# Kernel optimization log

Measured on AMD Instinct MI355X. Metric: run time of the kernel, lower is better.

Reference implementation:

```python
import jax, jax.numpy as jnp
import numpy as np

THETA = 10000.0

def _angles(h, w, fpt):
    # base_angles: theta^{-linspace(0,1,1+fpt//4)[:-1]}  -> (fpt//4,)
    powers = jnp.linspace(0.0, 1.0, 1 + fpt // 4)[:-1]
    base = jnp.power(THETA, -powers)
    x_mults = jnp.tile(jnp.arange(w, dtype=base.dtype), h)            # (N,)
    y_mults = jnp.repeat(jnp.arange(h, dtype=base.dtype), w)          # (N,)
    ang_x = x_mults[:, None] * base                                   # (N, fpt//4)
    ang_y = y_mults[:, None] * base                                   # (N, fpt//4)
    return jnp.concatenate([ang_x, ang_y], axis=1)                    # (N, fpt//2)


def _rotate(t, cos, sin):
    # t: (b, h, n, c) -> pairs (b, h, n, c//2, 2); standard 2D rotation per pair.
    b, hh, n, c = t.shape
    v = t.reshape(b, hh, n, c // 2, 2)
    v0, v1 = v[..., 0], v[..., 1]
    o0 = cos * v0 - sin * v1
    o1 = sin * v0 + cos * v1
    return jnp.stack([o0, o1], axis=-1).reshape(b, hh, n, c)


def setup_inputs() -> dict:
    key = jax.random.key(0)
    kq, kk = jax.random.split(key)
    b, heads, n, c = 4, 4, 4096, 256
    return {
        "q": jax.random.normal(kq, (b, heads, n, c), dtype=jnp.float32),
        "k": jax.random.normal(kk, (b, heads, n, c), dtype=jnp.float32),
        "h": 64,
        "w": 64,
    }


def reference(q, k, h, w):
    c = q.shape[-1]
    ang = _angles(h, w, c)            # (N, c//2)
    cos, sin = jnp.cos(ang), jnp.sin(ang)
    q_out = _rotate(q, cos, sin)
    k_out = _rotate(k, cos, sin)      # nk == nq here (no tiling branch)
    return q_out, k_out
```

## Files before the change

kernel.cpp:

```cpp
#include <hip/hip_runtime.h>

constexpr int B_ = 4, H_ = 4, N_ = 4096, C_ = 256;
constexpr long long TENS = (long long)B_ * H_ * N_ * C_;
constexpr int VEC = 4;
constexpr long long NTHREADS = TENS / VEC;
constexpr int F4_PER_POS = C_ / 4;
constexpr int TAB_ENTRIES = N_ * F4_PER_POS;
constexpr size_t TAB_BYTES = (size_t)TAB_ENTRIES * 16;

typedef float f32x4 __attribute__((ext_vector_type(4)));

__device__ __forceinline__ unsigned read_w(const int* __restrict__ wp) {
    int wi = wp[0];
    if (wi <= 0 || wi > 65536) {
        float wf = __int_as_float(wi);
        wi = (wf > 0.0f && wf <= 65536.0f) ? (int)wf : 64;
    }
    return (unsigned)wi;
}

__global__ __launch_bounds__(256) void build_tab_kernel(
    const int* __restrict__ wp, f32x4* __restrict__ tab)
{
    const unsigned idx = blockIdx.x * 256 + threadIdx.x;
    const unsigned w = read_w(wp);
    const unsigned pos = idx >> 6;
    const unsigned fq  = idx & 63;
    const unsigned x = pos % w;
    const unsigned y = pos / w;
    const float mult = (fq < 32) ? (float)x : (float)y;
    const int f0 = (int)(2u * (fq & 31u));
    constexpr float NEG_LOG2_THETA_OVER_64 = -0.20762050593045494f;
    float c0, s0, c1, s1;
    sincosf(mult * exp2f((float)f0       * NEG_LOG2_THETA_OVER_64), &s0, &c0);
    sincosf(mult * exp2f((float)(f0 + 1) * NEG_LOG2_THETA_OVER_64), &s1, &c1);
    f32x4 v; v.x = c0; v.y = s0; v.z = c1; v.w = s1;
    tab[idx] = v;
}

__global__ __launch_bounds__(256) void rope2d_tab_kernel(
    const f32x4* __restrict__ q4,
    const f32x4* __restrict__ k4,
    const f32x4* __restrict__ tab,
    f32x4* __restrict__ oq4,
    f32x4* __restrict__ ok4)
{
    const unsigned t = blockIdx.x * 256 + threadIdx.x;
    const f32x4 cs = tab[t & (unsigned)(TAB_ENTRIES - 1)];
    const f32x4 qa = __builtin_nontemporal_load(&q4[t]);
    const f32x4 ka = __builtin_nontemporal_load(&k4[t]);

    f32x4 r;
    r.x = fmaf(cs.x, qa.x, -cs.y * qa.y);
    r.y = fmaf(cs.y, qa.x,  cs.x * qa.y);
    r.z = fmaf(cs.z, qa.z, -cs.w * qa.w);
    r.w = fmaf(cs.w, qa.z,  cs.z * qa.w);
    __builtin_nontemporal_store(r, &oq4[t]);

    r.x = fmaf(cs.x, ka.x, -cs.y * ka.y);
    r.y = fmaf(cs.y, ka.x,  cs.x * ka.y);
    r.z = fmaf(cs.z, ka.z, -cs.w * ka.w);
    r.w = fmaf(cs.w, ka.z,  cs.z * ka.w);
    __builtin_nontemporal_store(r, &ok4[t]);
}

__global__ __launch_bounds__(256) void rope2d_inline_kernel(
    const float4* __restrict__ q4,
    const float4* __restrict__ k4,
    const int* __restrict__ wp,
    float4* __restrict__ oq4,
    float4* __restrict__ ok4)
{
    const unsigned w = read_w(wp);
    const unsigned t = blockIdx.x * 256 + threadIdx.x;
    const unsigned e = t * VEC;

    const int cidx = (int)(e & (C_ - 1));
    const unsigned pos = (e >> 8) & (N_ - 1);
    const unsigned x = pos % w;
    const unsigned y = pos / w;

    const int j0 = cidx >> 1;
    const float mult = (j0 < C_ / 4) ? (float)x : (float)y;
    const int f0 = j0 & (C_ / 4 - 1);

    float cs0, sn0, cs1, sn1;
    sincosf(mult * exp2f((float)(f0    ) * (-0.20762050593045494f)), &sn0, &cs0);
    sincosf(mult * exp2f((float)(f0 + 1) * (-0.20762050593045494f)), &sn1, &cs1);

    const float4 qa = q4[t];
    const float4 ka = k4[t];

    float4 r;
    r.x = fmaf(cs0, qa.x, -sn0 * qa.y);  r.y = fmaf(sn0, qa.x, cs0 * qa.y);
    r.z = fmaf(cs1, qa.z, -sn1 * qa.w);  r.w = fmaf(sn1, qa.z, cs1 * qa.w);
    oq4[t] = r;

    r.x = fmaf(cs0, ka.x, -sn0 * ka.y);  r.y = fmaf(sn0, ka.x, cs0 * ka.y);
    r.z = fmaf(cs1, ka.z, -sn1 * ka.w);  r.w = fmaf(sn1, ka.z, cs1 * ka.w);
    ok4[t] = r;
}

extern "C" void kernel_launch(void* const* d_in, const int* in_sizes, int n_in,
                              void* d_out, int out_size, void* d_ws, size_t ws_size,
                              hipStream_t stream) {
    const int* wp = (const int*)d_in[3];
    float* out = (float*)d_out;

    if (d_ws != nullptr && ws_size >= TAB_BYTES) {
        f32x4* tab = (f32x4*)d_ws;
        build_tab_kernel<<<dim3(TAB_ENTRIES / 256), 256, 0, stream>>>(wp, tab);
        rope2d_tab_kernel<<<dim3((unsigned)(NTHREADS / 256)), 256, 0, stream>>>(
            (const f32x4*)d_in[0], (const f32x4*)d_in[1], tab,
            (f32x4*)out, (f32x4*)(out + TENS));
    } else {
        rope2d_inline_kernel<<<dim3((unsigned)(NTHREADS / 256)), 256, 0, stream>>>(
            (const float4*)d_in[0], (const float4*)d_in[1], wp,
            (float4*)out, (float4*)(out + TENS));
    }
}
```

Baseline: 226.2 us.

## Fuse angle table build into rope kernel and loop over batch-heads

Replaces the two-kernel plan (build a cos/sin table in workspace, then apply it) with a single kernel. Each thread computes its cos/sin values in registers once and loops over all 16 batch-head slabs. This removes the table write and read traffic and one kernel launch. In exchange the grid shrinks 16x to 1024 blocks, which lowers the parallelism available to hide memory latency in this bandwidth-bound kernel.

Result: no change. 229.8 us (+1.6%).

```diff
diff --git a/kernel.cpp b/kernel.cpp
--- a/kernel.cpp
+++ b/kernel.cpp
@@ -2,11 +2,10 @@
 
 constexpr int B_ = 4, H_ = 4, N_ = 4096, C_ = 256;
 constexpr long long TENS = (long long)B_ * H_ * N_ * C_;
-constexpr int VEC = 4;
-constexpr long long NTHREADS = TENS / VEC;
+constexpr int BH = B_ * H_;
 constexpr int F4_PER_POS = C_ / 4;
-constexpr int TAB_ENTRIES = N_ * F4_PER_POS;
-constexpr size_t TAB_BYTES = (size_t)TAB_ENTRIES * 16;
+constexpr unsigned SLAB_F4 = (unsigned)(N_ * F4_PER_POS);
+constexpr unsigned NIDX = SLAB_F4;
 
 typedef float f32x4 __attribute__((ext_vector_type(4)));
 
@@ -19,8 +18,12 @@
     return (unsigned)wi;
 }
 
-__global__ __launch_bounds__(256) void build_tab_kernel(
-    const int* __restrict__ wp, f32x4* __restrict__ tab)
+__global__ __launch_bounds__(256) void rope2d_fused_kernel(
+    const f32x4* __restrict__ q4,
+    const f32x4* __restrict__ k4,
+    const int* __restrict__ wp,
+    f32x4* __restrict__ oq4,
+    f32x4* __restrict__ ok4)
 {
     const unsigned idx = blockIdx.x * 256 + threadIdx.x;
     const unsigned w = read_w(wp);
@@ -28,77 +31,34 @@
     const unsigned fq  = idx & 63;
     const unsigned x = pos % w;
     const unsigned y = pos / w;
+
     const float mult = (fq < 32) ? (float)x : (float)y;
     const int f0 = (int)(2u * (fq & 31u));
+
     constexpr float NEG_LOG2_THETA_OVER_64 = -0.20762050593045494f;
     float c0, s0, c1, s1;
     sincosf(mult * exp2f((float)f0       * NEG_LOG2_THETA_OVER_64), &s0, &c0);
     sincosf(mult * exp2f((float)(f0 + 1) * NEG_LOG2_THETA_OVER_64), &s1, &c1);
-    f32x4 v; v.x = c0; v.y = s0; v.z = c1; v.w = s1;
-    tab[idx] = v;
-}
 
-__global__ __launch_bounds__(256) void rope2d_tab_kernel(
-    const f32x4* __restrict__ q4,
-    const f32x4* __restrict__ k4,
-    const f32x4* __restrict__ tab,
-    f32x4* __restrict__ oq4,
-    f32x4* __restrict__ ok4)
-{
-    const unsigned t = blockIdx.x * 256 + threadIdx.x;
-    const f32x4 cs = tab[t & (unsigned)(TAB_ENTRIES - 1)];
-    const f32x4 qa = __builtin_nontemporal_load(&q4[t]);
-    const f32x4 ka = __builtin_nontemporal_load(&k4[t]);
+    #pragma unroll 4
+    for (int bh = 0; bh < BH; ++bh) {
+        const unsigned t = (unsigned)bh * SLAB_F4 + idx;
+        const f32x4 qa = __builtin_nontemporal_load(&q4[t]);
+        const f32x4 ka = __builtin_nontemporal_load(&k4[t]);
 
-    f32x4 r;
-    r.x = fmaf(cs.x, qa.x, -cs.y * qa.y);
-    r.y = fmaf(cs.y, qa.x,  cs.x * qa.y);
-    r.z = fmaf(cs.z, qa.z, -cs.w * qa.w);
-    r.w = fmaf(cs.w, qa.z,  cs.z * qa.w);
-    __builtin_nontemporal_store(r, &oq4[t]);
+        f32x4 r;
+        r.x = fmaf(c0, qa.x, -s0 * qa.y);
+        r.y = fmaf(s0, qa.x,  c0 * qa.y);
+        r.z = fmaf(c1, qa.z, -s1 * qa.w);
+        r.w = fmaf(s1, qa.z,  c1 * qa.w);
+        __builtin_nontemporal_store(r, &oq4[t]);
 
-    r.x = fmaf(cs.x, ka.x, -cs.y * ka.y);
-    r.y = fmaf(cs.y, ka.x,  cs.x * ka.y);
-    r.z = fmaf(cs.z, ka.z, -cs.w * ka.w);
-    r.w = fmaf(cs.w, ka.z,  cs.z * ka.w);
-    __builtin_nontemporal_store(r, &ok4[t]);
-}
-
-__global__ __launch_bounds__(256) void rope2d_inline_kernel(
-    const float4* __restrict__ q4,
-    const float4* __restrict__ k4,
-    const int* __restrict__ wp,
-    float4* __restrict__ oq4,
-    float4* __restrict__ ok4)
-{
-    const unsigned w = read_w(wp);
-    const unsigned t = blockIdx.x * 256 + threadIdx.x;
-    const unsigned e = t * VEC;
-
-    const int cidx = (int)(e & (C_ - 1));
-    const unsigned pos = (e >> 8) & (N_ - 1);
-    const unsigned x = pos % w;
-    const unsigned y = pos / w;
-
-    const int j0 = cidx >> 1;
-    const float mult = (j0 < C_ / 4) ? (float)x : (float)y;
-    const int f0 = j0 & (C_ / 4 - 1);
-
-    float cs0, sn0, cs1, sn1;
-    sincosf(mult * exp2f((float)(f0    ) * (-0.20762050593045494f)), &sn0, &cs0);
-    sincosf(mult * exp2f((float)(f0 + 1) * (-0.20762050593045494f)), &sn1, &cs1);
-
-    const float4 qa = q4[t];
-    const float4 ka = k4[t];
-
-    float4 r;
-    r.x = fmaf(cs0, qa.x, -sn0 * qa.y);  r.y = fmaf(sn0, qa.x, cs0 * qa.y);
-    r.z = fmaf(cs1, qa.z, -sn1 * qa.w);  r.w = fmaf(sn1, qa.z, cs1 * qa.w);
-    oq4[t] = r;
-
-    r.x = fmaf(cs0, ka.x, -sn0 * ka.y);  r.y = fmaf(sn0, ka.x, cs0 * ka.y);
-    r.z = fmaf(cs1, ka.z, -sn1 * ka.w);  r.w = fmaf(sn1, ka.z, cs1 * ka.w);
-    ok4[t] = r;
+        r.x = fmaf(c0, ka.x, -s0 * ka.y);
+        r.y = fmaf(s0, ka.x,  c0 * ka.y);
+        r.z = fmaf(c1, ka.z, -s1 * ka.w);
+        r.w = fmaf(s1, ka.z,  c1 * ka.w);
+        __builtin_nontemporal_store(r, &ok4[t]);
+    }
 }
 
 extern "C" void kernel_launch(void* const* d_in, const int* in_sizes, int n_in,
@@ -107,15 +67,7 @@
     const int* wp = (const int*)d_in[3];
     float* out = (float*)d_out;
 
-    if (d_ws != nullptr && ws_size >= TAB_BYTES) {
-        f32x4* tab = (f32x4*)d_ws;
-        build_tab_kernel<<<dim3(TAB_ENTRIES / 256), 256, 0, stream>>>(wp, tab);
-        rope2d_tab_kernel<<<dim3((unsigned)(NTHREADS / 256)), 256, 0, stream>>>(
-            (const f32x4*)d_in[0], (const f32x4*)d_in[1], tab,
-            (f32x4*)out, (f32x4*)(out + TENS));
-    } else {
-        rope2d_inline_kernel<<<dim3((unsigned)(NTHREADS / 256)), 256, 0, stream>>>(
-            (const float4*)d_in[0], (const float4*)d_in[1], wp,
-            (float4*)out, (float4*)(out + TENS));
-    }
+    rope2d_fused_kernel<<<dim3(NIDX / 256), 256, 0, stream>>>(
+        (const f32x4*)d_in[0], (const f32x4*)d_in[1], wp,
+        (f32x4*)out, (f32x4*)(out + TENS));
 }
```
